# Optimization experiments

Measured on AMD Instinct MI355X. Metric: run time of the kernel, lower is better.

## Reference

```python
import jax, jax.numpy as jnp
import numpy as np

NUM_SITES = 64
PHYS_DIM = 2
BOND_DIM = 32
BATCH = 65536


def _build_mps(num_sites, phys_dim, bond_dim, seed=0):
    """Replicates ImprovedMPS._initialize_tensors + _canonical_form, then
    zero-pads ragged cores into a dense [S, D, p, D] stack."""
    rng = np.random.default_rng(seed)
    tensors = []
    cur = 1
    for i in range(num_sites):
        if i == 0:
            nb = min(bond_dim, phys_dim)
            shape = (1, phys_dim, nb)
            cur = nb
        elif i == num_sites - 1:
            shape = (cur, phys_dim, 1)
        else:
            nb = min(bond_dim, cur * phys_dim)
            shape = (cur, phys_dim, nb)
            cur = nb
        ld, rd = shape[0] * shape[1], shape[2]
        m = (rng.standard_normal((ld, rd)) * 0.1).astype(np.float32)
        if ld >= rd:
            q, _ = np.linalg.qr(m)
            t = q.reshape(shape)
        else:
            q, _ = np.linalg.qr(m.T)
            t = q.T.reshape(shape)
        tensors.append(t.astype(np.float32))
    # left-canonical sweep
    for i in range(num_sites - 1):
        l, p, r = tensors[i].shape
        q, rr = np.linalg.qr(tensors[i].reshape(l * p, r))
        tensors[i] = q.reshape(l, p, q.shape[1]).astype(np.float32)
        nl, npd, nr = tensors[i + 1].shape
        tensors[i + 1] = (rr @ tensors[i + 1].reshape(nl, npd * nr)).reshape(rr.shape[0], npd, nr).astype(np.float32)
    # zero-pad ragged bonds into dense stack [S, D, p, D]
    A = np.zeros((num_sites, bond_dim, phys_dim, bond_dim), dtype=np.float32)
    for i, t in enumerate(tensors):
        l, p, r = t.shape
        A[i, :l, :, :r] = t
    return A


def setup_inputs() -> dict:
    key = jax.random.key(0)
    x_batch = jax.random.normal(key, (BATCH, NUM_SITES, PHYS_DIM), dtype=jnp.float32)
    A = jnp.asarray(_build_mps(NUM_SITES, PHYS_DIM, BOND_DIM))
    return {"x_batch": x_batch, "A": A}


def reference(x_batch, A):
    # x_batch: [B, S, p]; A: [S, D, p, D] (zero-padded ragged MPS cores)
    B = x_batch.shape[0]
    D = A.shape[1]
    # left_vector starts as ones(B,1) in the ragged view == one-hot e0 in padded view
    left0 = jnp.zeros((B, D), dtype=x_batch.dtype).at[:, 0].set(1.0)
    xs = jnp.moveaxis(x_batch, 1, 0)  # [S, B, p]

    def step(left, inp):
        A_i, x_i = inp  # [D, p, D], [B, p]
        # fuses: contracted = einsum('bp,lpd->bld'); left = einsum('bl,bld->bd')
        left = jnp.einsum('bl,bp,lpd->bd', left, x_i, A_i)
        return left, None

    left, _ = jax.lax.scan(step, left0, (A, xs))
    return left[:, :1]  # last core has right bond 1 -> only col 0 is nonzero
```

## Files before the change

### kernel.cpp

```cpp
#include <hip/hip_runtime.h>


typedef _Float16 half8 __attribute__((ext_vector_type(8)));
typedef float floatx4 __attribute__((ext_vector_type(4)));
typedef float f32x4 __attribute__((ext_vector_type(4)));

#define NSITES 64
#define CHUNK_ELEMS 16384

__global__ void mps_prep_afrag(const float* __restrict__ A, _Float16* __restrict__ Af) {
    __shared__ float sA[2048];
    const int site = blockIdx.x;
    const int tid  = threadIdx.x;
#pragma unroll
    for (int i = 0; i < 8; ++i) sA[tid + 256 * i] = A[site * 2048 + tid + 256 * i];
    __syncthreads();
    const int f     = tid >> 6;
    const int lane  = tid & 63;
    const int d     = 16 * (f >> 1) + (lane & 15);
    const int kbase = 32 * (f & 1) + (lane >> 4) * 8;
    half8 v;
#pragma unroll
    for (int e = 0; e < 8; ++e)
        v[e] = (_Float16)sA[(kbase + e) * 32 + d];
    reinterpret_cast<half8*>(Af)[(site * 4 + f) * 64 + lane] = v;
}

#define FRAGU(U, AC, X0, X1)                                                  \
    {                                                                         \
        float c0_ = AC[0], c1_ = AC[1], c2_ = AC[2], c3_ = AC[3];             \
        U[0] = (_Float16)(c0_ * (X0)); U[1] = (_Float16)(c0_ * (X1));         \
        U[2] = (_Float16)(c1_ * (X0)); U[3] = (_Float16)(c1_ * (X1));         \
        U[4] = (_Float16)(c2_ * (X0)); U[5] = (_Float16)(c2_ * (X1));         \
        U[6] = (_Float16)(c3_ * (X0)); U[7] = (_Float16)(c3_ * (X1));         \
    }

#define STEP(SL, AI0, AI1, AO0, AO1, XB, J)                                   \
    {                                                                         \
        const float x0_ = XB[2 * (J)], x1_ = XB[2 * (J) + 1];                 \
        half8 u0_, u1_;                                                       \
        FRAGU(u0_, AI0, x0_, x1_);                                            \
        FRAGU(u1_, AI1, x0_, x1_);                                            \
        AO0 = __builtin_amdgcn_mfma_f32_16x16x32_f16(SL[0], u0_, zv, 0, 0, 0);   \
        AO1 = __builtin_amdgcn_mfma_f32_16x16x32_f16(SL[2], u0_, zv, 0, 0, 0);   \
        AO0 = __builtin_amdgcn_mfma_f32_16x16x32_f16(SL[1], u1_, AO0, 0, 0, 0);  \
        AO1 = __builtin_amdgcn_mfma_f32_16x16x32_f16(SL[3], u1_, AO1, 0, 0, 0);  \
    }

#define RDFRAG(DST, BUF, S)                                                   \
    {                                                                         \
        _Pragma("unroll")                                                     \
        for (int f_ = 0; f_ < 4; ++f_)                                        \
            DST[f_] = *(const half8*)&smA[BUF][(((S) * 4 + f_) * 64 + lane) * 8]; \
    }

#define STAGE(C, BUF)                                                         \
    {                                                                         \
        _Pragma("unroll")                                                     \
        for (int r_ = 0; r_ < 4; ++r_) {                                      \
            const int rec_ = r_ * 8 + wid;                                    \
            const _Float16* g_ = Af + (size_t)(C) * CHUNK_ELEMS + rec_ * 512 + lane * 8; \
            __builtin_amdgcn_global_load_lds(                                 \
                (const __attribute__((address_space(1))) void*)g_,            \
                (__attribute__((address_space(3))) void*)&smA[BUF][rec_ * 512], \
                16, 0, 0);                                                    \
        }                                                                     \
    }

#define LOADX(DST, OCT)                                                       \
    {                                                                         \
        f32x4 t0_ = xp[(OCT) * 4 + 0];                                        \
        f32x4 t1_ = xp[(OCT) * 4 + 1];                                        \
        f32x4 t2_ = xp[(OCT) * 4 + 2];                                        \
        f32x4 t3_ = xp[(OCT) * 4 + 3];                                        \
        DST[0]  = t0_[0]; DST[1]  = t0_[1]; DST[2]  = t0_[2]; DST[3]  = t0_[3]; \
        DST[4]  = t1_[0]; DST[5]  = t1_[1]; DST[6]  = t1_[2]; DST[7]  = t1_[3]; \
        DST[8]  = t2_[0]; DST[9]  = t2_[1]; DST[10] = t2_[2]; DST[11] = t2_[3]; \
        DST[12] = t3_[0]; DST[13] = t3_[1]; DST[14] = t3_[2]; DST[15] = t3_[3]; \
    }

#define CHUNK_BODY(C, BUF, XCUR, XNEXT, DO_NEXT)                              \
    {                                                                         \
        if (DO_NEXT) { STAGE((C) + 1, 1 - (BUF)); LOADX(XNEXT, (C) + 1); }    \
        STEP(F0, a0, a1, n0, n1, XCUR, 0) RDFRAG(F0, BUF, 2)                  \
        STEP(F1, n0, n1, a0, a1, XCUR, 1) RDFRAG(F1, BUF, 3)                  \
        STEP(F0, a0, a1, n0, n1, XCUR, 2) RDFRAG(F0, BUF, 4)                  \
        STEP(F1, n0, n1, a0, a1, XCUR, 3) RDFRAG(F1, BUF, 5)                  \
        STEP(F0, a0, a1, n0, n1, XCUR, 4) RDFRAG(F0, BUF, 6)                  \
        STEP(F1, n0, n1, a0, a1, XCUR, 5) RDFRAG(F1, BUF, 7)                  \
        STEP(F0, a0, a1, n0, n1, XCUR, 6)                                     \
        STEP(F1, n0, n1, a0, a1, XCUR, 7)                                     \
        __syncthreads();                                                      \
        if (DO_NEXT) { RDFRAG(F0, 1 - (BUF), 0) RDFRAG(F1, 1 - (BUF), 1) }    \
    }

__global__ __launch_bounds__(512, 4) void mps_main(const float* __restrict__ x,
                                                   const _Float16* __restrict__ Af,
                                                   float* __restrict__ out) {
    __shared__ __align__(16) _Float16 smA[2][CHUNK_ELEMS];

    const int lane = threadIdx.x & 63;
    const int wid  = threadIdx.x >> 6;
    const int row0 = (blockIdx.x * 8 + wid) * 16;
    const int b    = row0 + (lane & 15);

    const f32x4* xp = reinterpret_cast<const f32x4*>(x + (size_t)b * (NSITES * 2));

    floatx4 zv;
#pragma unroll
    for (int i = 0; i < 4; ++i) zv[i] = 0.f;

    floatx4 a0, a1, n0, n1;
#pragma unroll
    for (int i = 0; i < 4; ++i) { a0[i] = 0.f; a1[i] = 0.f; n0[i] = 0.f; n1[i] = 0.f; }
    if (lane < 16) a0[0] = 1.f;

    float xa[16], xb2[16];
    half8 F0[4], F1[4];

    STAGE(0, 0);
    LOADX(xa, 0);
    __syncthreads();
    RDFRAG(F0, 0, 0)
    RDFRAG(F1, 0, 1)

    CHUNK_BODY(0, 0, xa,  xb2, 1)
    CHUNK_BODY(1, 1, xb2, xa,  1)
    CHUNK_BODY(2, 0, xa,  xb2, 1)
    CHUNK_BODY(3, 1, xb2, xa,  1)
    CHUNK_BODY(4, 0, xa,  xb2, 1)
    CHUNK_BODY(5, 1, xb2, xa,  1)
    CHUNK_BODY(6, 0, xa,  xb2, 1)
    CHUNK_BODY(7, 1, xb2, xa,  0)

    if (lane < 16) out[row0 + lane] = a0[0];
}

extern "C" void kernel_launch(void* const* d_in, const int* in_sizes, int n_in,
                              void* d_out, int out_size, void* d_ws, size_t ws_size,
                              hipStream_t stream) {
    const float* x = (const float*)d_in[0];
    const float* A = (const float*)d_in[1];
    float* outp = (float*)d_out;
    _Float16* Af = (_Float16*)d_ws;

    hipLaunchKernelGGL(mps_prep_afrag, dim3(NSITES), dim3(256), 0, stream, A, Af);
    hipLaunchKernelGGL(mps_main, dim3(65536 / 128), dim3(512), 0, stream, x, Af, outp);
}
```

Before: 35.78 us.

## Pipeline MPS sites across waves with register-resident cores and LDS bond handoff

Replaces the design where each wave runs all 64 sites for its own 16 rows, streaming A fragments through LDS. Each wave now holds 8 sites' A fragments in registers and processes a stream of 16-row tiles as a systolic pipeline, passing bond vectors to the next wave through padded LDS buffers. The aim is to remove per-chunk A staging and LDS fragment reads. In exchange there are pipeline fill and drain bubbles (23 stages for 16 tiles), a block barrier per stage, narrower 8-byte x loads, and fewer blocks (256 instead of 512), which lowers parallelism.

```diff
diff --git a/kernel.cpp b/kernel.cpp
--- a/kernel.cpp
+++ b/kernel.cpp
@@ -3,10 +3,15 @@
 
 typedef _Float16 half8 __attribute__((ext_vector_type(8)));
 typedef float floatx4 __attribute__((ext_vector_type(4)));
-typedef float f32x4 __attribute__((ext_vector_type(4)));
+typedef float f32x2 __attribute__((ext_vector_type(2)));
 
 #define NSITES 64
-#define CHUNK_ELEMS 16384
+#define WAVES 8
+#define SPW 8
+#define TILE 16
+#define TILES 16
+#define RSTRIDE 36
+#define BNDSZ (TILE * RSTRIDE)
 
 __global__ void mps_prep_afrag(const float* __restrict__ A, _Float16* __restrict__ Af) {
     __shared__ float sA[2048];
@@ -28,112 +33,105 @@
 
 #define FRAGU(U, AC, X0, X1)                                                  \
     {                                                                         \
-        float c0_ = AC[0], c1_ = AC[1], c2_ = AC[2], c3_ = AC[3];             \
-        U[0] = (_Float16)(c0_ * (X0)); U[1] = (_Float16)(c0_ * (X1));         \
-        U[2] = (_Float16)(c1_ * (X0)); U[3] = (_Float16)(c1_ * (X1));         \
-        U[4] = (_Float16)(c2_ * (X0)); U[5] = (_Float16)(c2_ * (X1));         \
-        U[6] = (_Float16)(c3_ * (X0)); U[7] = (_Float16)(c3_ * (X1));         \
+        U[0] = (_Float16)(AC[0] * (X0)); U[1] = (_Float16)(AC[0] * (X1));     \
+        U[2] = (_Float16)(AC[1] * (X0)); U[3] = (_Float16)(AC[1] * (X1));     \
+        U[4] = (_Float16)(AC[2] * (X0)); U[5] = (_Float16)(AC[2] * (X1));     \
+        U[6] = (_Float16)(AC[3] * (X0)); U[7] = (_Float16)(AC[3] * (X1));     \
     }
 
-#define STEP(SL, AI0, AI1, AO0, AO1, XB, J)                                   \
+#define SITE(S, AI0, AI1, AO0, AO1, XB)                                       \
     {                                                                         \
-        const float x0_ = XB[2 * (J)], x1_ = XB[2 * (J) + 1];                 \
+        const float x0_ = XB[S][0], x1_ = XB[S][1];                           \
         half8 u0_, u1_;                                                       \
         FRAGU(u0_, AI0, x0_, x1_);                                            \
         FRAGU(u1_, AI1, x0_, x1_);                                            \
-        AO0 = __builtin_amdgcn_mfma_f32_16x16x32_f16(SL[0], u0_, zv, 0, 0, 0);   \
-        AO1 = __builtin_amdgcn_mfma_f32_16x16x32_f16(SL[2], u0_, zv, 0, 0, 0);   \
-        AO0 = __builtin_amdgcn_mfma_f32_16x16x32_f16(SL[1], u1_, AO0, 0, 0, 0);  \
-        AO1 = __builtin_amdgcn_mfma_f32_16x16x32_f16(SL[3], u1_, AO1, 0, 0, 0);  \
+        AO0 = __builtin_amdgcn_mfma_f32_16x16x32_f16(AF[S][0], u0_, zv, 0, 0, 0);   \
+        AO1 = __builtin_amdgcn_mfma_f32_16x16x32_f16(AF[S][2], u0_, zv, 0, 0, 0);   \
+        AO0 = __builtin_amdgcn_mfma_f32_16x16x32_f16(AF[S][1], u1_, AO0, 0, 0, 0);  \
+        AO1 = __builtin_amdgcn_mfma_f32_16x16x32_f16(AF[S][3], u1_, AO1, 0, 0, 0);  \
     }
 
-#define RDFRAG(DST, BUF, S)                                                   \
+#define BODY(T, PAR, XCUR, XNXT)                                              \
     {                                                                         \
-        _Pragma("unroll")                                                     \
-        for (int f_ = 0; f_ < 4; ++f_)                                        \
-            DST[f_] = *(const half8*)&smA[BUF][(((S) * 4 + f_) * 64 + lane) * 8]; \
+        const int tt_  = (T) - wid;                                           \
+        const int ntt_ = (T) + 1 - wid;                                       \
+        if (0 <= ntt_ && ntt_ < TILES) {                                      \
+            const float* xb_ = x + ((size_t)(row0 + ntt_ * TILE + row)) * 128 \
+                                 + wid * 16;                                  \
+            _Pragma("unroll")                                                 \
+            for (int s_ = 0; s_ < SPW; ++s_)                                  \
+                XNXT[s_] = *(const f32x2*)(xb_ + 2 * s_);                     \
+        }                                                                     \
+        if (0 <= tt_ && tt_ < TILES) {                                        \
+            floatx4 L0, L1, c0, c1, d0, d1;                                   \
+            if (wid == 0) {                                                   \
+                L0 = zv; L1 = zv;                                             \
+                if (lane < 16) L0[0] = 1.f;                   \
+            } else {                                                          \
+                const float* rp_ = &st[(((PAR) ^ 1) * WAVES + wid) * BNDSZ    \
+                                       + row * RSTRIDE];                      \
+                L0 = *(const floatx4*)(rp_ + g4);                             \
+                L1 = *(const floatx4*)(rp_ + 16 + g4);                        \
+            }                                                                 \
+            SITE(0, L0, L1, c0, c1, XCUR)                                     \
+            SITE(1, c0, c1, d0, d1, XCUR)                                     \
+            SITE(2, d0, d1, c0, c1, XCUR)                                     \
+            SITE(3, c0, c1, d0, d1, XCUR)                                     \
+            SITE(4, d0, d1, c0, c1, XCUR)                                     \
+            SITE(5, c0, c1, d0, d1, XCUR)                                     \
+            SITE(6, d0, d1, c0, c1, XCUR)                                     \
+            SITE(7, c0, c1, d0, d1, XCUR)                                     \
+            if (wid < WAVES - 1) {                                            \
+                float* wp_ = &st[((PAR) * WAVES + wid + 1) * BNDSZ            \
+                                 + row * RSTRIDE];                            \
+                *(floatx4*)(wp_ + g4)      = d0;                              \
+                *(floatx4*)(wp_ + 16 + g4) = d1;                              \
+            } else if (lane < 16) {                                           \
+                out[row0 + tt_ * TILE + lane] = d0[0];                        \
+            }                                                                 \
+        }                                                                     \
+        __syncthreads();                                                      \
     }
 
-#define STAGE(C, BUF)                                                         \
-    {                                                                         \
-        _Pragma("unroll")                                                     \
-        for (int r_ = 0; r_ < 4; ++r_) {                                      \
-            const int rec_ = r_ * 8 + wid;                                    \
-            const _Float16* g_ = Af + (size_t)(C) * CHUNK_ELEMS + rec_ * 512 + lane * 8; \
-            __builtin_amdgcn_global_load_lds(                                 \
-                (const __attribute__((address_space(1))) void*)g_,            \
-                (__attribute__((address_space(3))) void*)&smA[BUF][rec_ * 512], \
-                16, 0, 0);                                                    \
-        }                                                                     \
-    }
-
-#define LOADX(DST, OCT)                                                       \
-    {                                                                         \
-        f32x4 t0_ = xp[(OCT) * 4 + 0];                                        \
-        f32x4 t1_ = xp[(OCT) * 4 + 1];                                        \
-        f32x4 t2_ = xp[(OCT) * 4 + 2];                                        \
-        f32x4 t3_ = xp[(OCT) * 4 + 3];                                        \
-        DST[0]  = t0_[0]; DST[1]  = t0_[1]; DST[2]  = t0_[2]; DST[3]  = t0_[3]; \
-        DST[4]  = t1_[0]; DST[5]  = t1_[1]; DST[6]  = t1_[2]; DST[7]  = t1_[3]; \
-        DST[8]  = t2_[0]; DST[9]  = t2_[1]; DST[10] = t2_[2]; DST[11] = t2_[3]; \
-        DST[12] = t3_[0]; DST[13] = t3_[1]; DST[14] = t3_[2]; DST[15] = t3_[3]; \
-    }
-
-#define CHUNK_BODY(C, BUF, XCUR, XNEXT, DO_NEXT)                              \
-    {                                                                         \
-        if (DO_NEXT) { STAGE((C) + 1, 1 - (BUF)); LOADX(XNEXT, (C) + 1); }    \
-        STEP(F0, a0, a1, n0, n1, XCUR, 0) RDFRAG(F0, BUF, 2)                  \
-        STEP(F1, n0, n1, a0, a1, XCUR, 1) RDFRAG(F1, BUF, 3)                  \
-        STEP(F0, a0, a1, n0, n1, XCUR, 2) RDFRAG(F0, BUF, 4)                  \
-        STEP(F1, n0, n1, a0, a1, XCUR, 3) RDFRAG(F1, BUF, 5)                  \
-        STEP(F0, a0, a1, n0, n1, XCUR, 4) RDFRAG(F0, BUF, 6)                  \
-        STEP(F1, n0, n1, a0, a1, XCUR, 5) RDFRAG(F1, BUF, 7)                  \
-        STEP(F0, a0, a1, n0, n1, XCUR, 6)                                     \
-        STEP(F1, n0, n1, a0, a1, XCUR, 7)                                     \
-        __syncthreads();                                                      \
-        if (DO_NEXT) { RDFRAG(F0, 1 - (BUF), 0) RDFRAG(F1, 1 - (BUF), 1) }    \
-    }
-
-__global__ __launch_bounds__(512, 4) void mps_main(const float* __restrict__ x,
-                                                   const _Float16* __restrict__ Af,
-                                                   float* __restrict__ out) {
-    __shared__ __align__(16) _Float16 smA[2][CHUNK_ELEMS];
+__global__ __launch_bounds__(512) void mps_main(const float* __restrict__ x,
+                                                const _Float16* __restrict__ Af,
+                                                float* __restrict__ out) {
+    __shared__ float st[2 * WAVES * BNDSZ];
 
     const int lane = threadIdx.x & 63;
     const int wid  = threadIdx.x >> 6;
-    const int row0 = (blockIdx.x * 8 + wid) * 16;
-    const int b    = row0 + (lane & 15);
+    const int row  = lane & 15;
+    const int g4   = (lane >> 4) * 4;
+    const int row0 = blockIdx.x * (TILES * TILE);
 
-    const f32x4* xp = reinterpret_cast<const f32x4*>(x + (size_t)b * (NSITES * 2));
+    const half8* ap = reinterpret_cast<const half8*>(Af);
 
     floatx4 zv;
 #pragma unroll
     for (int i = 0; i < 4; ++i) zv[i] = 0.f;
 
-    floatx4 a0, a1, n0, n1;
+    half8 AF[SPW][4];
 #pragma unroll
-    for (int i = 0; i < 4; ++i) { a0[i] = 0.f; a1[i] = 0.f; n0[i] = 0.f; n1[i] = 0.f; }
-    if (lane < 16) a0[0] = 1.f;
+    for (int s = 0; s < SPW; ++s)
+#pragma unroll
+        for (int f = 0; f < 4; ++f)
+            AF[s][f] = ap[((wid * SPW + s) * 4 + f) * 64 + lane];
 
-    float xa[16], xb2[16];
-    half8 F0[4], F1[4];
+    f32x2 xa[SPW], xb[SPW];
+#pragma unroll
+    for (int s = 0; s < SPW; ++s) { xa[s][0] = 0.f; xa[s][1] = 0.f; }
+    if (wid == 0) {
+        const float* xb0 = x + ((size_t)(row0 + row)) * 128 + wid * 16;
+#pragma unroll
+        for (int s = 0; s < SPW; ++s) xa[s] = *(const f32x2*)(xb0 + 2 * s);
+    }
+    __syncthreads();
 
-    STAGE(0, 0);
-    LOADX(xa, 0);
-    __syncthreads();
-    RDFRAG(F0, 0, 0)
-    RDFRAG(F1, 0, 1)
-
-    CHUNK_BODY(0, 0, xa,  xb2, 1)
-    CHUNK_BODY(1, 1, xb2, xa,  1)
-    CHUNK_BODY(2, 0, xa,  xb2, 1)
-    CHUNK_BODY(3, 1, xb2, xa,  1)
-    CHUNK_BODY(4, 0, xa,  xb2, 1)
-    CHUNK_BODY(5, 1, xb2, xa,  1)
-    CHUNK_BODY(6, 0, xa,  xb2, 1)
-    CHUNK_BODY(7, 1, xb2, xa,  0)
-
-    if (lane < 16) out[row0 + lane] = a0[0];
+    for (int it = 0; it < 12; ++it) {
+        const int t0 = 2 * it;
+        BODY(t0,     0, xa, xb)
+        BODY(t0 + 1, 1, xb, xa)
+    }
 }
 
 extern "C" void kernel_launch(void* const* d_in, const int* in_sizes, int n_in,
@@ -145,5 +143,5 @@
     _Float16* Af = (_Float16*)d_ws;
 
     hipLaunchKernelGGL(mps_prep_afrag, dim3(NSITES), dim3(256), 0, stream, A, Af);
-    hipLaunchKernelGGL(mps_main, dim3(65536 / 128), dim3(512), 0, stream, x, Af, outp);
+    hipLaunchKernelGGL(mps_main, dim3(65536 / (TILES * TILE)), dim3(512), 0, stream, x, Af, outp);
 }
```

After: 55.48 us. +55.0%, slower.

## Process two interleaved 16-row batch tiles per wave to reuse A fragments

Applied to the files above, without the earlier changes.

Each wave now advances two independent 16-row batch tiles through the MPS chain, so every A fragment read from LDS feeds two sets of MFMAs. The second chain also gives the scheduler independent work to hide MFMA dependency latency. Blocks shrink to 4 waves, so each wave stages twice as many A records, and x is loaded in small per-pair pieces rather than 16-float octets. This costs more registers per thread for the duplicated accumulators and lowers the per-block wave count.

```diff
diff --git a/kernel.cpp b/kernel.cpp
--- a/kernel.cpp
+++ b/kernel.cpp
@@ -28,24 +28,31 @@
 
 #define FRAGU(U, AC, X0, X1)                                                  \
     {                                                                         \
-        float c0_ = AC[0], c1_ = AC[1], c2_ = AC[2], c3_ = AC[3];             \
-        U[0] = (_Float16)(c0_ * (X0)); U[1] = (_Float16)(c0_ * (X1));         \
-        U[2] = (_Float16)(c1_ * (X0)); U[3] = (_Float16)(c1_ * (X1));         \
-        U[4] = (_Float16)(c2_ * (X0)); U[5] = (_Float16)(c2_ * (X1));         \
-        U[6] = (_Float16)(c3_ * (X0)); U[7] = (_Float16)(c3_ * (X1));         \
+        U[0] = (_Float16)(AC[0] * (X0)); U[1] = (_Float16)(AC[0] * (X1));     \
+        U[2] = (_Float16)(AC[1] * (X0)); U[3] = (_Float16)(AC[1] * (X1));     \
+        U[4] = (_Float16)(AC[2] * (X0)); U[5] = (_Float16)(AC[2] * (X1));     \
+        U[6] = (_Float16)(AC[3] * (X0)); U[7] = (_Float16)(AC[3] * (X1));     \
     }
 
-#define STEP(SL, AI0, AI1, AO0, AO1, XB, J)                                   \
+#define MFMA16(A_, B_, C_) __builtin_amdgcn_mfma_f32_16x16x32_f16(A_, B_, C_, 0, 0, 0)
+
+#define SITE(SL, I00, I01, I10, I11, O00, O01, O10, O11, XT0, XT1, J)         \
     {                                                                         \
-        const float x0_ = XB[2 * (J)], x1_ = XB[2 * (J) + 1];                 \
-        half8 u0_, u1_;                                                       \
-        FRAGU(u0_, AI0, x0_, x1_);                                            \
-        FRAGU(u1_, AI1, x0_, x1_);                                            \
-        AO0 = __builtin_amdgcn_mfma_f32_16x16x32_f16(SL[0], u0_, zv, 0, 0, 0);   \
-        AO1 = __builtin_amdgcn_mfma_f32_16x16x32_f16(SL[2], u0_, zv, 0, 0, 0);   \
-        AO0 = __builtin_amdgcn_mfma_f32_16x16x32_f16(SL[1], u1_, AO0, 0, 0, 0);  \
-        AO1 = __builtin_amdgcn_mfma_f32_16x16x32_f16(SL[3], u1_, AO1, 0, 0, 0);  \
+        const float p0_ = XT0[2 * (J)], p1_ = XT0[2 * (J) + 1];               \
+        const float q0_ = XT1[2 * (J)], q1_ = XT1[2 * (J) + 1];               \
+        half8 u00_, u01_, u10_, u11_;                                         \
+        FRAGU(u00_, I00, p0_, p1_);                                           \
+        FRAGU(u01_, I01, p0_, p1_);                                           \
+        FRAGU(u10_, I10, q0_, q1_);                                           \
+        FRAGU(u11_, I11, q0_, q1_);                                           \
+        O00 = MFMA16(SL[0], u00_, zv);  O01 = MFMA16(SL[2], u00_, zv);        \
+        O10 = MFMA16(SL[0], u10_, zv);  O11 = MFMA16(SL[2], u10_, zv);        \
+        O00 = MFMA16(SL[1], u01_, O00); O01 = MFMA16(SL[3], u01_, O01);       \
+        O10 = MFMA16(SL[1], u11_, O10); O11 = MFMA16(SL[3], u11_, O11);       \
     }
+
+#define SITE_E(SL, XT0, XT1, J) SITE(SL, pa0, pa1, qa0, qa1, pn0, pn1, qn0, qn1, XT0, XT1, J)
+#define SITE_O(SL, XT0, XT1, J) SITE(SL, pn0, pn1, qn0, qn1, pa0, pa1, qa0, qa1, XT0, XT1, J)
 
 #define RDFRAG(DST, BUF, S)                                                   \
     {                                                                         \
@@ -57,8 +64,8 @@
 #define STAGE(C, BUF)                                                         \
     {                                                                         \
         _Pragma("unroll")                                                     \
-        for (int r_ = 0; r_ < 4; ++r_) {                                      \
-            const int rec_ = r_ * 8 + wid;                                    \
+        for (int r_ = 0; r_ < 8; ++r_) {                                      \
+            const int rec_ = r_ * 4 + wid;                                    \
             const _Float16* g_ = Af + (size_t)(C) * CHUNK_ELEMS + rec_ * 512 + lane * 8; \
             __builtin_amdgcn_global_load_lds(                                 \
                 (const __attribute__((address_space(1))) void*)g_,            \
@@ -67,73 +74,82 @@
         }                                                                     \
     }
 
-#define LOADX(DST, OCT)                                                       \
+#define LOADP(DA, DB, P)                                                      \
     {                                                                         \
-        f32x4 t0_ = xp[(OCT) * 4 + 0];                                        \
-        f32x4 t1_ = xp[(OCT) * 4 + 1];                                        \
-        f32x4 t2_ = xp[(OCT) * 4 + 2];                                        \
-        f32x4 t3_ = xp[(OCT) * 4 + 3];                                        \
-        DST[0]  = t0_[0]; DST[1]  = t0_[1]; DST[2]  = t0_[2]; DST[3]  = t0_[3]; \
-        DST[4]  = t1_[0]; DST[5]  = t1_[1]; DST[6]  = t1_[2]; DST[7]  = t1_[3]; \
-        DST[8]  = t2_[0]; DST[9]  = t2_[1]; DST[10] = t2_[2]; DST[11] = t2_[3]; \
-        DST[12] = t3_[0]; DST[13] = t3_[1]; DST[14] = t3_[2]; DST[15] = t3_[3]; \
+        f32x4 ta_ = xp0[(P) & 31];                                            \
+        f32x4 tb_ = xp1[(P) & 31];                                            \
+        DA[0] = ta_[0]; DA[1] = ta_[1]; DA[2] = ta_[2]; DA[3] = ta_[3];       \
+        DB[0] = tb_[0]; DB[1] = tb_[1]; DB[2] = tb_[2]; DB[3] = tb_[3];       \
     }
 
-#define CHUNK_BODY(C, BUF, XCUR, XNEXT, DO_NEXT)                              \
+#define CHUNK(C, BUF, DO_NEXT)                                                \
     {                                                                         \
-        if (DO_NEXT) { STAGE((C) + 1, 1 - (BUF)); LOADX(XNEXT, (C) + 1); }    \
-        STEP(F0, a0, a1, n0, n1, XCUR, 0) RDFRAG(F0, BUF, 2)                  \
-        STEP(F1, n0, n1, a0, a1, XCUR, 1) RDFRAG(F1, BUF, 3)                  \
-        STEP(F0, a0, a1, n0, n1, XCUR, 2) RDFRAG(F0, BUF, 4)                  \
-        STEP(F1, n0, n1, a0, a1, XCUR, 3) RDFRAG(F1, BUF, 5)                  \
-        STEP(F0, a0, a1, n0, n1, XCUR, 4) RDFRAG(F0, BUF, 6)                  \
-        STEP(F1, n0, n1, a0, a1, XCUR, 5) RDFRAG(F1, BUF, 7)                  \
-        STEP(F0, a0, a1, n0, n1, XCUR, 6)                                     \
-        STEP(F1, n0, n1, a0, a1, XCUR, 7)                                     \
+        if (DO_NEXT) STAGE((C) + 1, 1 - (BUF));                               \
+        LOADP(xB0, xB1, 4 * (C) + 1)                                          \
+        SITE_E(F0, xA0, xA1, 0) RDFRAG(F0, BUF, 2)                            \
+        SITE_O(F1, xA0, xA1, 1) RDFRAG(F1, BUF, 3)                            \
+        LOADP(xA0, xA1, 4 * (C) + 2)                                          \
+        SITE_E(F0, xB0, xB1, 0) RDFRAG(F0, BUF, 4)                            \
+        SITE_O(F1, xB0, xB1, 1) RDFRAG(F1, BUF, 5)                            \
+        LOADP(xB0, xB1, 4 * (C) + 3)                                          \
+        SITE_E(F0, xA0, xA1, 0) RDFRAG(F0, BUF, 6)                            \
+        SITE_O(F1, xA0, xA1, 1) RDFRAG(F1, BUF, 7)                            \
+        LOADP(xA0, xA1, 4 * (C) + 4)                                          \
+        SITE_E(F0, xB0, xB1, 0)                                               \
+        SITE_O(F1, xB0, xB1, 1)                                               \
         __syncthreads();                                                      \
         if (DO_NEXT) { RDFRAG(F0, 1 - (BUF), 0) RDFRAG(F1, 1 - (BUF), 1) }    \
     }
 
-__global__ __launch_bounds__(512, 4) void mps_main(const float* __restrict__ x,
+__global__ __launch_bounds__(256, 2) void mps_main(const float* __restrict__ x,
                                                    const _Float16* __restrict__ Af,
                                                    float* __restrict__ out) {
     __shared__ __align__(16) _Float16 smA[2][CHUNK_ELEMS];
 
-    const int lane = threadIdx.x & 63;
-    const int wid  = threadIdx.x >> 6;
-    const int row0 = (blockIdx.x * 8 + wid) * 16;
-    const int b    = row0 + (lane & 15);
+    const int lane  = threadIdx.x & 63;
+    const int wid   = threadIdx.x >> 6;
+    const int wbase = (blockIdx.x * 4 + wid) * 32;
+    const int r     = lane & 15;
+    const int b0    = wbase + r;
+    const int b1    = wbase + 16 + r;
 
-    const f32x4* xp = reinterpret_cast<const f32x4*>(x + (size_t)b * (NSITES * 2));
+    const f32x4* xp0 = reinterpret_cast<const f32x4*>(x + (size_t)b0 * (NSITES * 2));
+    const f32x4* xp1 = reinterpret_cast<const f32x4*>(x + (size_t)b1 * (NSITES * 2));
 
     floatx4 zv;
 #pragma unroll
     for (int i = 0; i < 4; ++i) zv[i] = 0.f;
 
-    floatx4 a0, a1, n0, n1;
+    floatx4 pa0, pa1, qa0, qa1, pn0, pn1, qn0, qn1;
 #pragma unroll
-    for (int i = 0; i < 4; ++i) { a0[i] = 0.f; a1[i] = 0.f; n0[i] = 0.f; n1[i] = 0.f; }
-    if (lane < 16) a0[0] = 1.f;
+    for (int i = 0; i < 4; ++i) {
+        pa0[i] = 0.f; pa1[i] = 0.f; qa0[i] = 0.f; qa1[i] = 0.f;
+        pn0[i] = 0.f; pn1[i] = 0.f; qn0[i] = 0.f; qn1[i] = 0.f;
+    }
+    if (lane < 16) { pa0[0] = 1.f; qa0[0] = 1.f; }
 
-    float xa[16], xb2[16];
+    float xA0[4], xA1[4], xB0[4], xB1[4];
     half8 F0[4], F1[4];
 
     STAGE(0, 0);
-    LOADX(xa, 0);
+    LOADP(xA0, xA1, 0)
     __syncthreads();
     RDFRAG(F0, 0, 0)
     RDFRAG(F1, 0, 1)
 
-    CHUNK_BODY(0, 0, xa,  xb2, 1)
-    CHUNK_BODY(1, 1, xb2, xa,  1)
-    CHUNK_BODY(2, 0, xa,  xb2, 1)
-    CHUNK_BODY(3, 1, xb2, xa,  1)
-    CHUNK_BODY(4, 0, xa,  xb2, 1)
-    CHUNK_BODY(5, 1, xb2, xa,  1)
-    CHUNK_BODY(6, 0, xa,  xb2, 1)
-    CHUNK_BODY(7, 1, xb2, xa,  0)
+    CHUNK(0, 0, 1)
+    CHUNK(1, 1, 1)
+    CHUNK(2, 0, 1)
+    CHUNK(3, 1, 1)
+    CHUNK(4, 0, 1)
+    CHUNK(5, 1, 1)
+    CHUNK(6, 0, 1)
+    CHUNK(7, 1, 0)
 
-    if (lane < 16) out[row0 + lane] = a0[0];
+    if (lane < 16) {
+        out[wbase + lane]      = pa0[0];
+        out[wbase + 16 + lane] = qa0[0];
+    }
 }
 
 extern "C" void kernel_launch(void* const* d_in, const int* in_sizes, int n_in,
@@ -145,5 +161,5 @@
     _Float16* Af = (_Float16*)d_ws;
 
     hipLaunchKernelGGL(mps_prep_afrag, dim3(NSITES), dim3(256), 0, stream, A, Af);
-    hipLaunchKernelGGL(mps_main, dim3(65536 / 128), dim3(512), 0, stream, x, Af, outp);
+    hipLaunchKernelGGL(mps_main, dim3(65536 / 128), dim3(256), 0, stream, x, Af, outp);
 }
```

Measured after the change: 40.08 us. +12.0%, slower.
